# Performance work log

Hardware: AMD Instinct MI355X
Metric: run time of the kernel (lower is better)

The kernel has to match this reference:

```python
import jax, jax.numpy as jnp
import numpy as np

D_MODEL = 1024
N_HEAD = 16
D_K = D_MODEL // N_HEAD
D_FF = 2048
EPS = 1e-6
SCALE = np.sqrt(D_K).astype(np.float32)


def layer_norm(x, alpha, beta):
    # Faithful to source: unbiased std (ddof=1), eps added to std
    mean = jnp.mean(x, axis=-1, keepdims=True)
    std = jnp.std(x, axis=-1, keepdims=True, ddof=1) + EPS
    return alpha * (x - mean) / std + beta


def setup_inputs() -> dict:
    key = jax.random.key(0)
    ks = jax.random.split(key, 12)
    s = 0.02
    return {
        "x": jax.random.normal(ks[0], (4, 1024, D_MODEL), dtype=jnp.float32),
        "Wq": jax.random.normal(ks[1], (D_MODEL, D_MODEL), dtype=jnp.float32) * s,
        "bq": jax.random.normal(ks[2], (D_MODEL,), dtype=jnp.float32) * s,
        "Wo": jax.random.normal(ks[3], (D_MODEL, D_MODEL), dtype=jnp.float32) * s,
        "bo": jax.random.normal(ks[4], (D_MODEL,), dtype=jnp.float32) * s,
        "W1": jax.random.normal(ks[5], (D_MODEL, D_FF), dtype=jnp.float32) * s,
        "b1": jax.random.normal(ks[6], (D_FF,), dtype=jnp.float32) * s,
        "W2": jax.random.normal(ks[7], (D_FF, D_MODEL), dtype=jnp.float32) * s,
        "b2": jax.random.normal(ks[8], (D_MODEL,), dtype=jnp.float32) * s,
        "alpha": jnp.ones((D_MODEL,), dtype=jnp.float32),
        "beta": jnp.ones((D_MODEL,), dtype=jnp.float32),
    }


def reference(x, Wq, bq, Wo, bo, W1, b1, W2, b2, alpha, beta):
    b, s, d = x.shape
    # Source bug kept: q, k, v all use q_linear
    def proj(t):
        return (t @ Wq + bq).reshape(b, s, N_HEAD, D_K).transpose(0, 2, 1, 3)
    q = proj(x)  # [b,h,s,dk]
    k = proj(x)
    v = proj(x)
    scores = jnp.einsum('bhqd,bhkd->bhqk', q, k) / SCALE
    scores = jax.nn.softmax(scores, axis=-1)
    z = jnp.einsum('bhqk,bhkd->bhqd', scores, v)
    concat = z.transpose(0, 2, 1, 3).reshape(b, s, d)
    attn_out = concat @ Wo + bo
    x = layer_norm(x + attn_out, alpha, beta)
    ff = jax.nn.relu(x @ W1 + b1) @ W2 + b2
    x = layer_norm(x + ff, alpha, beta)  # source reuses norm_1
    return x
```

## Files before the change

kernel.cpp:

```cpp
#include <hip/hip_runtime.h>
#include <hip/hip_bf16.h>
#include <stdint.h>

#define TOK   4096
#define DMODEL 1024
#define DFF    2048
#define NHEAD  16
#define DK     64

typedef unsigned short u16;
typedef __attribute__((ext_vector_type(8))) short short8;
typedef __attribute__((ext_vector_type(4))) float f32x4;

typedef __attribute__((address_space(1))) void gvoid;
typedef __attribute__((address_space(3))) void lvoid;

#define QSCALE   0.35355339f
#define QUNSCALE 2.82842712f

__device__ __forceinline__ u16 f2b(float f) {
    uint32_t x = __builtin_bit_cast(uint32_t, f);
    x += 0x7FFFu + ((x >> 16) & 1u);
    return (u16)(x >> 16);
}
__device__ __forceinline__ float b2f(u16 u) {
    uint32_t x = ((uint32_t)u) << 16;
    return __builtin_bit_cast(float, x);
}

__device__ __forceinline__ void gload16(const void* g, void* l) {
    __builtin_amdgcn_global_load_lds((gvoid*)g, (lvoid*)l, 16, 0, 0);
}

__global__ __launch_bounds__(256) void cvt_bf16_k(
    const float* __restrict__ in, u16* __restrict__ out, int n4)
{
    int i = blockIdx.x * 256 + threadIdx.x;
    if (i >= n4) return;
    float4 v = ((const float4*)in)[i];
    ushort4 o;
    o.x = f2b(v.x); o.y = f2b(v.y); o.z = f2b(v.z); o.w = f2b(v.w);
    ((ushort4*)out)[i] = o;
}

__global__ __launch_bounds__(256) void cvt_tr_k(
    const float* __restrict__ W, u16* __restrict__ Wt, int K, int N)
{
    __shared__ u16 T[64][68];
    const int tx = threadIdx.x & 15, ty = threadIdx.x >> 4;
    const int n0 = blockIdx.x * 64, k0 = blockIdx.y * 64;
#pragma unroll
    for (int i = 0; i < 4; i++) {
        int k = ty + i * 16;
        float4 v = *(const float4*)&W[(size_t)(k0 + k) * N + n0 + tx * 4];
        T[tx * 4 + 0][k] = f2b(v.x);
        T[tx * 4 + 1][k] = f2b(v.y);
        T[tx * 4 + 2][k] = f2b(v.z);
        T[tx * 4 + 3][k] = f2b(v.w);
    }
    __syncthreads();
#pragma unroll
    for (int i = 0; i < 4; i++) {
        int n = ty + i * 16;
        ushort4 o;
        o.x = T[n][tx * 4 + 0]; o.y = T[n][tx * 4 + 1];
        o.z = T[n][tx * 4 + 2]; o.w = T[n][tx * 4 + 3];
        *(ushort4*)&Wt[(size_t)(n0 + n) * K + k0 + tx * 4] = o;
    }
}

template<bool RELU, bool OUTBF16, bool QOUT>
__global__ __launch_bounds__(256) void gemm_mfma(
    const u16* __restrict__ A, const u16* __restrict__ Bt,
    const float* __restrict__ bias, void* __restrict__ Cv,
    u16* __restrict__ CT, float oscale,
    int M, int N, int K)
{
    __shared__ __align__(16) u16 As[2 * 128 * 64];
    __shared__ __align__(16) u16 Bs[2 * 128 * 64];

    const int tid  = threadIdx.x;
    const int lane = tid & 63;
    const int wid  = tid >> 6;
    const int wm = wid >> 1, wn = wid & 1;
    const int frow = lane & 15, fk = lane >> 4;

    const int gx = N >> 7;
    const int L = blockIdx.x;
    const int xcd = L & 7, within = L >> 3;
    const int yy = xcd * 4 + within / gx;
    const int xx = within % gx;

    const int row0 = yy * 128;
    const int col0 = xx * 128;

    const u16* gA[4]; u16* lA[4];
    const u16* gB[4]; u16* lB[4];
#pragma unroll
    for (int inst = 0; inst < 4; inst++) {
        int s = inst * 256 + tid;
        int r = s >> 3;
        int kc = ((s & 7) ^ (r & 7)) * 8;
        gA[inst] = A  + (size_t)(row0 + r) * K + kc;
        gB[inst] = Bt + (size_t)(col0 + r) * K + kc;
        lA[inst] = As + inst * 2048 + wid * 512;
        lB[inst] = Bs + inst * 2048 + wid * 512;
    }

    int aoff[4][2], boff[4][2];
#pragma unroll
    for (int m = 0; m < 4; m++) {
        int r = wm * 64 + m * 16 + frow;
#pragma unroll
        for (int kk = 0; kk < 2; kk++)
            aoff[m][kk] = r * 64 + (((kk << 2) + fk) ^ (r & 7)) * 8;
    }
#pragma unroll
    for (int n = 0; n < 4; n++) {
        int r = wn * 64 + n * 16 + frow;
#pragma unroll
        for (int kk = 0; kk < 2; kk++)
            boff[n][kk] = r * 64 + (((kk << 2) + fk) ^ (r & 7)) * 8;
    }

    f32x4 acc[4][4] = {};
    const int nT = K >> 6;

#pragma unroll
    for (int inst = 0; inst < 4; inst++) {
        gload16(gA[inst], lA[inst]);
        gload16(gB[inst], lB[inst]);
    }
    __syncthreads();

    for (int t = 0; t < nT; t++) {
        const int cur = t & 1;
        if (t + 1 < nT) {
            const int k0 = (t + 1) << 6;
            const int bo = (cur ^ 1) * 8192;
#pragma unroll
            for (int inst = 0; inst < 4; inst++) {
                gload16(gA[inst] + k0, lA[inst] + bo);
                gload16(gB[inst] + k0, lB[inst] + bo);
            }
        }

        const u16* Ab = As + cur * 8192;
        const u16* Bb = Bs + cur * 8192;
        short8 a[4][2], b[4][2];
#pragma unroll
        for (int m = 0; m < 4; m++)
#pragma unroll
            for (int kk = 0; kk < 2; kk++)
                a[m][kk] = *(const short8*)(Ab + aoff[m][kk]);
#pragma unroll
        for (int n = 0; n < 4; n++)
#pragma unroll
            for (int kk = 0; kk < 2; kk++)
                b[n][kk] = *(const short8*)(Bb + boff[n][kk]);

#pragma unroll
        for (int m = 0; m < 4; m++)
#pragma unroll
            for (int n = 0; n < 4; n++)
#pragma unroll
                for (int kk = 0; kk < 2; kk++)
                    acc[m][n] = __builtin_amdgcn_mfma_f32_16x16x32_bf16(
                        a[m][kk], b[n][kk], acc[m][n], 0, 0, 0);

        __syncthreads();
    }

#pragma unroll
    for (int n = 0; n < 4; n++) {
        const int gcol = col0 + wn * 64 + n * 16 + frow;
        const float bv = bias[gcol];
#pragma unroll
        for (int m = 0; m < 4; m++) {
            const int grow0 = row0 + wm * 64 + m * 16 + fk * 4;
            float v[4];
#pragma unroll
            for (int i = 0; i < 4; i++) {
                v[i] = (acc[m][n][i] + bv) * oscale;
                if (RELU) v[i] = fmaxf(v[i], 0.0f);
                if (OUTBF16)
                    ((u16*)Cv)[(size_t)(grow0 + i) * N + gcol] = f2b(v[i]);
                else
                    ((float*)Cv)[(size_t)(grow0 + i) * N + gcol] = v[i];
            }
            if (QOUT) {
                const int hh = gcol >> 6, d = gcol & 63;
                const int bb = grow0 >> 10, sl = grow0 & 1023;
                ushort4 o;
                o.x = f2b(v[0]); o.y = f2b(v[1]); o.z = f2b(v[2]); o.w = f2b(v[3]);
                *(ushort4*)&CT[(((size_t)(bb * 16 + hh) * 64 + d) << 10) + sl] = o;
            }
        }
    }
}

__global__ __launch_bounds__(256, 2) void attn_mfma(
    const u16* __restrict__ qb, const u16* __restrict__ qT,
    u16* __restrict__ zb)
{
    __shared__ __align__(16) u16 Ks[2][64 * 64];
    __shared__ __align__(16) u16 Kt[2][64 * 64];
    __shared__ __align__(16) u16 Ps[128 * 64];

    const int tid  = threadIdx.x;
    const int lane = tid & 63;
    const int w    = tid >> 6;
    const int frow = lane & 15, fk = lane >> 4;

    const int h  = blockIdx.x;
    const int qt = blockIdx.y;
    const int b  = blockIdx.z;
    const int q0 = qt * 128;

    const u16* qhead = qb + ((size_t)b * 1024) * 1024 + h * 64;
    const u16* thead = qT + ((size_t)(b * 16 + h) * 64) * 1024;

#pragma unroll
    for (int inst = 0; inst < 2; inst++) {
        int s = inst * 256 + tid, r = s >> 3, kc = ((s & 7) ^ (r & 7)) * 8;
        gload16(qhead + (size_t)r * 1024 + kc, Ks[0] + inst * 2048 + w * 512);
        gload16(thead + (size_t)r * 1024 + kc, Kt[0] + inst * 2048 + w * 512);
    }

    short8 qf[2][2];
#pragma unroll
    for (int m = 0; m < 2; m++) {
        int r = q0 + w * 32 + m * 16 + frow;
#pragma unroll
        for (int kk = 0; kk < 2; kk++)
            qf[m][kk] = *(const short8*)(qhead + (size_t)r * 1024 + kk * 32 + fk * 8);
    }

    float lp[2] = {};
    f32x4 o[2][4] = {};

    __syncthreads();

    for (int t = 0; t < 16; t++) {
        const int cur = t & 1;
        if (t < 15) {
            const int kv = (t + 1) * 64;
#pragma unroll
            for (int inst = 0; inst < 2; inst++) {
                int s = inst * 256 + tid, r = s >> 3, kc = ((s & 7) ^ (r & 7)) * 8;
                gload16(qhead + (size_t)(kv + r) * 1024 + kc,
                        Ks[cur ^ 1] + inst * 2048 + w * 512);
                gload16(thead + (size_t)r * 1024 + kv + kc,
                        Kt[cur ^ 1] + inst * 2048 + w * 512);
            }
        }

        short8 kf[4][2];
#pragma unroll
        for (int n = 0; n < 4; n++) {
            int r = n * 16 + frow;
#pragma unroll
            for (int kk = 0; kk < 2; kk++)
                kf[n][kk] = *(const short8*)(Ks[cur] + r * 64 +
                                             (((kk << 2) + fk) ^ (r & 7)) * 8);
        }
        f32x4 st[4][2] = {};
#pragma unroll
        for (int nk = 0; nk < 4; nk++)
#pragma unroll
            for (int mq = 0; mq < 2; mq++)
#pragma unroll
                for (int kk = 0; kk < 2; kk++)
                    st[nk][mq] = __builtin_amdgcn_mfma_f32_16x16x32_bf16(
                        kf[nk][kk], qf[mq][kk], st[nk][mq], 0, 0, 0);

#pragma unroll
        for (int mq = 0; mq < 2; mq++) {
            const int r = w * 32 + mq * 16 + frow;
            const int rb = r * 64, sw = (r & 7) << 3;
#pragma unroll
            for (int nk = 0; nk < 4; nk++) {
                ushort4 pb;
                float p0 = __expf(st[nk][mq][0]);
                float p1 = __expf(st[nk][mq][1]);
                float p2 = __expf(st[nk][mq][2]);
                float p3 = __expf(st[nk][mq][3]);
                lp[mq] += (p0 + p1) + (p2 + p3);
                pb.x = f2b(p0); pb.y = f2b(p1); pb.z = f2b(p2); pb.w = f2b(p3);
                *(ushort4*)&Ps[rb + ((nk * 16 + fk * 4) ^ sw)] = pb;
            }
        }

        short8 pa[2][2], vf[4][2];
#pragma unroll
        for (int m = 0; m < 2; m++) {
            int r = w * 32 + m * 16 + frow;
#pragma unroll
            for (int kk = 0; kk < 2; kk++)
                pa[m][kk] = *(const short8*)(Ps + r * 64 +
                                             (((kk << 2) + fk) ^ (r & 7)) * 8);
        }
#pragma unroll
        for (int n = 0; n < 4; n++) {
            int r = n * 16 + frow;
#pragma unroll
            for (int kk = 0; kk < 2; kk++)
                vf[n][kk] = *(const short8*)(Kt[cur] + r * 64 +
                                             (((kk << 2) + fk) ^ (r & 7)) * 8);
        }
#pragma unroll
        for (int m = 0; m < 2; m++)
#pragma unroll
            for (int n = 0; n < 4; n++)
#pragma unroll
                for (int kk = 0; kk < 2; kk++)
                    o[m][n] = __builtin_amdgcn_mfma_f32_16x16x32_bf16(
                        pa[m][kk], vf[n][kk], o[m][n], 0, 0, 0);

        __syncthreads();
    }

#pragma unroll
    for (int mq = 0; mq < 2; mq++) {
        lp[mq] += __shfl_xor(lp[mq], 16);
        lp[mq] += __shfl_xor(lp[mq], 32);
    }
#pragma unroll
    for (int m = 0; m < 2; m++)
#pragma unroll
        for (int i = 0; i < 4; i++) {
            const float lfull = __shfl(lp[m], fk * 4 + i);
            const float rl = QUNSCALE / lfull;
            const size_t gr = (size_t)(b * 1024 + q0 + w * 32 + m * 16 + fk * 4 + i);
#pragma unroll
            for (int n = 0; n < 4; n++)
                zb[gr * 1024 + h * 64 + n * 16 + frow] = f2b(o[m][n][i] * rl);
        }
}

__device__ __forceinline__ float ldval(const float* p) { return *p; }
__device__ __forceinline__ float ldval(const u16* p)   { return b2f(*p); }
__device__ __forceinline__ void  stval(float* p, float v) { *p = v; }
__device__ __forceinline__ void  stval(u16* p, float v)   { *p = f2b(v); }

template<typename TA, typename TB, typename TO>
__global__ __launch_bounds__(256) void add_ln(
    const TA* __restrict__ a, const TB* __restrict__ b,
    const float* __restrict__ alpha, const float* __restrict__ beta,
    TO* __restrict__ out)
{
    const int row = blockIdx.x;
    const TA* ar = a + (size_t)row * DMODEL;
    const TB* br = b + (size_t)row * DMODEL;

    float v[4];
    float sum = 0.0f, sq = 0.0f;
#pragma unroll
    for (int i = 0; i < 4; i++) {
        int c = threadIdx.x + i * 256;
        v[i] = ldval(ar + c) + ldval(br + c);
        sum += v[i];
        sq  += v[i] * v[i];
    }
#pragma unroll
    for (int off = 32; off > 0; off >>= 1) {
        sum += __shfl_xor(sum, off);
        sq  += __shfl_xor(sq, off);
    }
    __shared__ float s1[4], s2[4];
    const int wid = threadIdx.x >> 6, lane = threadIdx.x & 63;
    if (lane == 0) { s1[wid] = sum; s2[wid] = sq; }
    __syncthreads();
    sum = s1[0] + s1[1] + s1[2] + s1[3];
    sq  = s2[0] + s2[1] + s2[2] + s2[3];

    const float mean = sum * (1.0f / 1024.0f);
    float var = (sq - 1024.0f * mean * mean) * (1.0f / 1023.0f);
    var = fmaxf(var, 0.0f);
    const float rdenom = 1.0f / (sqrtf(var) + 1e-6f);

#pragma unroll
    for (int i = 0; i < 4; i++) {
        int c = threadIdx.x + i * 256;
        stval(out + (size_t)row * DMODEL + c,
              alpha[c] * (v[i] - mean) * rdenom + beta[c]);
    }
}

extern "C" void kernel_launch(void* const* d_in, const int* in_sizes, int n_in,
                              void* d_out, int out_size, void* d_ws, size_t ws_size,
                              hipStream_t stream) {
    const float* x     = (const float*)d_in[0];
    const float* Wq    = (const float*)d_in[1];
    const float* bq    = (const float*)d_in[2];
    const float* Wo    = (const float*)d_in[3];
    const float* bo    = (const float*)d_in[4];
    const float* W1    = (const float*)d_in[5];
    const float* b1    = (const float*)d_in[6];
    const float* W2    = (const float*)d_in[7];
    const float* b2    = (const float*)d_in[8];
    const float* alpha = (const float*)d_in[9];
    const float* beta  = (const float*)d_in[10];

    char* base = (char*)d_ws;
    u16* Wqt = (u16*)base;
    u16* Wot = (u16*)(base + (2u  << 20));
    u16* W1t = (u16*)(base + (4u  << 20));
    u16* W2t = (u16*)(base + (8u  << 20));
    u16* zb  = (u16*)(base + (12u << 20));
    u16* x1b = zb;
    u16* qb  = (u16*)(base + (20u << 20));
    u16* qT  = (u16*)(base + (28u << 20));
    u16* xb  = (u16*)(base + (36u << 20));
    float* g  = (float*)(base + (36u << 20));
    u16*  hb  = (u16*)g;
    float* g2 = (float*)(base + (20u << 20));

    dim3 blk(256);

    cvt_tr_k<<<dim3(16, 16), blk, 0, stream>>>(Wq, Wqt, 1024, 1024);
    cvt_tr_k<<<dim3(16, 16), blk, 0, stream>>>(Wo, Wot, 1024, 1024);
    cvt_tr_k<<<dim3(32, 16), blk, 0, stream>>>(W1, W1t, 1024, 2048);
    cvt_tr_k<<<dim3(16, 32), blk, 0, stream>>>(W2, W2t, 2048, 1024);
    cvt_bf16_k<<<dim3(TOK * DMODEL / 4 / 256), blk, 0, stream>>>(x, xb, TOK * DMODEL / 4);

    gemm_mfma<false, true, true><<<dim3(8 * 32), blk, 0, stream>>>(
        xb, Wqt, bq, qb, qT, QSCALE, TOK, 1024, 1024);
    attn_mfma<<<dim3(16, 8, 4), blk, 0, stream>>>(qb, qT, zb);
    gemm_mfma<false, false, false><<<dim3(8 * 32), blk, 0, stream>>>(
        zb, Wot, bo, g, nullptr, 1.0f, TOK, 1024, 1024);
    add_ln<float, float, u16><<<dim3(TOK), blk, 0, stream>>>(x, g, alpha, beta, x1b);
    gemm_mfma<true, true, false><<<dim3(16 * 32), blk, 0, stream>>>(
        x1b, W1t, b1, hb, nullptr, 1.0f, TOK, 2048, 1024);
    gemm_mfma<false, false, false><<<dim3(8 * 32), blk, 0, stream>>>(
        hb, W2t, b2, g2, nullptr, 1.0f, TOK, 1024, 2048);
    add_ln<u16, float, float><<<dim3(TOK), blk, 0, stream>>>(
        x1b, g2, alpha, beta, (float*)d_out);
}
```

Baseline: 170.4 us.

## Merge prep kernels, use 128x64 GEMM tiles, bf16 GEMM outputs, vectorize LayerNorm

```diff
diff --git a/kernel.cpp b/kernel.cpp
--- a/kernel.cpp
+++ b/kernel.cpp
@@ -27,28 +27,20 @@
     uint32_t x = ((uint32_t)u) << 16;
     return __builtin_bit_cast(float, x);
 }
+__device__ __forceinline__ uint32_t f2b2(float lo, float hi) {
+    return (uint32_t)f2b(lo) | ((uint32_t)f2b(hi) << 16);
+}
 
 __device__ __forceinline__ void gload16(const void* g, void* l) {
     __builtin_amdgcn_global_load_lds((gvoid*)g, (lvoid*)l, 16, 0, 0);
 }
 
-__global__ __launch_bounds__(256) void cvt_bf16_k(
-    const float* __restrict__ in, u16* __restrict__ out, int n4)
+__device__ __forceinline__ void cvt_tr_dev(
+    const float* __restrict__ W, u16* __restrict__ Wt, int K, int N,
+    int bx, int by, int tid, u16 T[64][68])
 {
-    int i = blockIdx.x * 256 + threadIdx.x;
-    if (i >= n4) return;
-    float4 v = ((const float4*)in)[i];
-    ushort4 o;
-    o.x = f2b(v.x); o.y = f2b(v.y); o.z = f2b(v.z); o.w = f2b(v.w);
-    ((ushort4*)out)[i] = o;
-}
-
-__global__ __launch_bounds__(256) void cvt_tr_k(
-    const float* __restrict__ W, u16* __restrict__ Wt, int K, int N)
-{
-    __shared__ u16 T[64][68];
-    const int tx = threadIdx.x & 15, ty = threadIdx.x >> 4;
-    const int n0 = blockIdx.x * 64, k0 = blockIdx.y * 64;
+    const int tx = tid & 15, ty = tid >> 4;
+    const int n0 = bx * 64, k0 = by * 64;
 #pragma unroll
     for (int i = 0; i < 4; i++) {
         int k = ty + i * 16;
@@ -69,15 +61,48 @@
     }
 }
 
-template<bool RELU, bool OUTBF16, bool QOUT>
+__global__ __launch_bounds__(256) void prep_all(
+    const float* __restrict__ Wq, const float* __restrict__ Wo,
+    const float* __restrict__ W1, const float* __restrict__ W2,
+    u16* __restrict__ Wqt, u16* __restrict__ Wot,
+    u16* __restrict__ W1t, u16* __restrict__ W2t,
+    const float* __restrict__ x, u16* __restrict__ xb)
+{
+    __shared__ u16 T[64][68];
+    const int id = blockIdx.x, tid = threadIdx.x;
+    if (id < 256) {
+        cvt_tr_dev(Wq, Wqt, 1024, 1024, id & 15, id >> 4, tid, T);
+    } else if (id < 512) {
+        int t = id - 256;
+        cvt_tr_dev(Wo, Wot, 1024, 1024, t & 15, t >> 4, tid, T);
+    } else if (id < 1024) {
+        int t = id - 512;
+        cvt_tr_dev(W1, W1t, 1024, 2048, t & 31, t >> 5, tid, T);
+    } else if (id < 1536) {
+        int t = id - 1024;
+        cvt_tr_dev(W2, W2t, 2048, 1024, t & 15, t >> 4, tid, T);
+    } else {
+        size_t base = (size_t)(id - 1536) * 1024 + tid;
+#pragma unroll
+        for (int j = 0; j < 4; j++) {
+            float4 v = ((const float4*)x)[base + j * 256];
+            ((uint2*)xb)[base + j * 256] =
+                make_uint2(f2b2(v.x, v.y), f2b2(v.z, v.w));
+        }
+    }
+}
+
+template<int BN, bool RELU, bool OUTBF16, bool QOUT>
 __global__ __launch_bounds__(256) void gemm_mfma(
     const u16* __restrict__ A, const u16* __restrict__ Bt,
     const float* __restrict__ bias, void* __restrict__ Cv,
     u16* __restrict__ CT, float oscale,
     int M, int N, int K)
 {
+    constexpr int NF = BN / 32;
+    constexpr int BSTR = BN * 64;
     __shared__ __align__(16) u16 As[2 * 128 * 64];
-    __shared__ __align__(16) u16 Bs[2 * 128 * 64];
+    __shared__ __align__(16) u16 Bs[2 * BSTR];
 
     const int tid  = threadIdx.x;
     const int lane = tid & 63;
@@ -85,29 +110,35 @@
     const int wm = wid >> 1, wn = wid & 1;
     const int frow = lane & 15, fk = lane >> 4;
 
-    const int gx = N >> 7;
+    const int gx = N / BN;
     const int L = blockIdx.x;
     const int xcd = L & 7, within = L >> 3;
     const int yy = xcd * 4 + within / gx;
     const int xx = within % gx;
 
     const int row0 = yy * 128;
-    const int col0 = xx * 128;
+    const int col0 = xx * BN;
 
     const u16* gA[4]; u16* lA[4];
-    const u16* gB[4]; u16* lB[4];
+    const u16* gB[NF]; u16* lB[NF];
 #pragma unroll
     for (int inst = 0; inst < 4; inst++) {
         int s = inst * 256 + tid;
         int r = s >> 3;
         int kc = ((s & 7) ^ (r & 7)) * 8;
-        gA[inst] = A  + (size_t)(row0 + r) * K + kc;
+        gA[inst] = A + (size_t)(row0 + r) * K + kc;
+        lA[inst] = As + inst * 2048 + wid * 512;
+    }
+#pragma unroll
+    for (int inst = 0; inst < NF; inst++) {
+        int s = inst * 256 + tid;
+        int r = s >> 3;
+        int kc = ((s & 7) ^ (r & 7)) * 8;
         gB[inst] = Bt + (size_t)(col0 + r) * K + kc;
-        lA[inst] = As + inst * 2048 + wid * 512;
         lB[inst] = Bs + inst * 2048 + wid * 512;
     }
 
-    int aoff[4][2], boff[4][2];
+    int aoff[4][2], boff[NF][2];
 #pragma unroll
     for (int m = 0; m < 4; m++) {
         int r = wm * 64 + m * 16 + frow;
@@ -116,45 +147,44 @@
             aoff[m][kk] = r * 64 + (((kk << 2) + fk) ^ (r & 7)) * 8;
     }
 #pragma unroll
-    for (int n = 0; n < 4; n++) {
-        int r = wn * 64 + n * 16 + frow;
+    for (int n = 0; n < NF; n++) {
+        int r = wn * (BN / 2) + n * 16 + frow;
 #pragma unroll
         for (int kk = 0; kk < 2; kk++)
             boff[n][kk] = r * 64 + (((kk << 2) + fk) ^ (r & 7)) * 8;
     }
 
-    f32x4 acc[4][4] = {};
+    f32x4 acc[4][NF] = {};
     const int nT = K >> 6;
 
 #pragma unroll
-    for (int inst = 0; inst < 4; inst++) {
-        gload16(gA[inst], lA[inst]);
-        gload16(gB[inst], lB[inst]);
-    }
+    for (int inst = 0; inst < 4; inst++) gload16(gA[inst], lA[inst]);
+#pragma unroll
+    for (int inst = 0; inst < NF; inst++) gload16(gB[inst], lB[inst]);
     __syncthreads();
 
     for (int t = 0; t < nT; t++) {
         const int cur = t & 1;
         if (t + 1 < nT) {
             const int k0 = (t + 1) << 6;
-            const int bo = (cur ^ 1) * 8192;
-#pragma unroll
-            for (int inst = 0; inst < 4; inst++) {
-                gload16(gA[inst] + k0, lA[inst] + bo);
-                gload16(gB[inst] + k0, lB[inst] + bo);
-            }
+#pragma unroll
+            for (int inst = 0; inst < 4; inst++)
+                gload16(gA[inst] + k0, lA[inst] + (cur ^ 1) * 8192);
+#pragma unroll
+            for (int inst = 0; inst < NF; inst++)
+                gload16(gB[inst] + k0, lB[inst] + (cur ^ 1) * BSTR);
         }
 
         const u16* Ab = As + cur * 8192;
-        const u16* Bb = Bs + cur * 8192;
-        short8 a[4][2], b[4][2];
+        const u16* Bb = Bs + cur * BSTR;
+        short8 a[4][2], b[NF][2];
 #pragma unroll
         for (int m = 0; m < 4; m++)
 #pragma unroll
             for (int kk = 0; kk < 2; kk++)
                 a[m][kk] = *(const short8*)(Ab + aoff[m][kk]);
 #pragma unroll
-        for (int n = 0; n < 4; n++)
+        for (int n = 0; n < NF; n++)
 #pragma unroll
             for (int kk = 0; kk < 2; kk++)
                 b[n][kk] = *(const short8*)(Bb + boff[n][kk]);
@@ -162,7 +192,7 @@
 #pragma unroll
         for (int m = 0; m < 4; m++)
 #pragma unroll
-            for (int n = 0; n < 4; n++)
+            for (int n = 0; n < NF; n++)
 #pragma unroll
                 for (int kk = 0; kk < 2; kk++)
                     acc[m][n] = __builtin_amdgcn_mfma_f32_16x16x32_bf16(
@@ -172,8 +202,8 @@
     }
 
 #pragma unroll
-    for (int n = 0; n < 4; n++) {
-        const int gcol = col0 + wn * 64 + n * 16 + frow;
+    for (int n = 0; n < NF; n++) {
+        const int gcol = col0 + wn * (BN / 2) + n * 16 + frow;
         const float bv = bias[gcol];
 #pragma unroll
         for (int m = 0; m < 4; m++) {
@@ -191,9 +221,8 @@
             if (QOUT) {
                 const int hh = gcol >> 6, d = gcol & 63;
                 const int bb = grow0 >> 10, sl = grow0 & 1023;
-                ushort4 o;
-                o.x = f2b(v[0]); o.y = f2b(v[1]); o.z = f2b(v[2]); o.w = f2b(v[3]);
-                *(ushort4*)&CT[(((size_t)(bb * 16 + hh) * 64 + d) << 10) + sl] = o;
+                *(uint2*)&CT[(((size_t)(bb * 16 + hh) * 64 + d) << 10) + sl] =
+                    make_uint2(f2b2(v[0], v[1]), f2b2(v[2], v[3]));
             }
         }
     }
@@ -280,14 +309,13 @@
             const int rb = r * 64, sw = (r & 7) << 3;
 #pragma unroll
             for (int nk = 0; nk < 4; nk++) {
-                ushort4 pb;
                 float p0 = __expf(st[nk][mq][0]);
                 float p1 = __expf(st[nk][mq][1]);
                 float p2 = __expf(st[nk][mq][2]);
                 float p3 = __expf(st[nk][mq][3]);
                 lp[mq] += (p0 + p1) + (p2 + p3);
-                pb.x = f2b(p0); pb.y = f2b(p1); pb.z = f2b(p2); pb.w = f2b(p3);
-                *(ushort4*)&Ps[rb + ((nk * 16 + fk * 4) ^ sw)] = pb;
+                *(uint2*)&Ps[rb + ((nk * 16 + fk * 4) ^ sw)] =
+                    make_uint2(f2b2(p0, p1), f2b2(p2, p3));
             }
         }
 
@@ -338,10 +366,15 @@
         }
 }
 
-__device__ __forceinline__ float ldval(const float* p) { return *p; }
-__device__ __forceinline__ float ldval(const u16* p)   { return b2f(*p); }
-__device__ __forceinline__ void  stval(float* p, float v) { *p = v; }
-__device__ __forceinline__ void  stval(u16* p, float v)   { *p = f2b(v); }
+__device__ __forceinline__ float4 ld4(const float* p) { return *(const float4*)p; }
+__device__ __forceinline__ float4 ld4(const u16* p) {
+    ushort4 u = *(const ushort4*)p;
+    return make_float4(b2f(u.x), b2f(u.y), b2f(u.z), b2f(u.w));
+}
+__device__ __forceinline__ void st4(float* p, float4 v) { *(float4*)p = v; }
+__device__ __forceinline__ void st4(u16* p, float4 v) {
+    *(uint2*)p = make_uint2(f2b2(v.x, v.y), f2b2(v.z, v.w));
+}
 
 template<typename TA, typename TB, typename TO>
 __global__ __launch_bounds__(256) void add_ln(
@@ -350,18 +383,14 @@
     TO* __restrict__ out)
 {
     const int row = blockIdx.x;
-    const TA* ar = a + (size_t)row * DMODEL;
-    const TB* br = b + (size_t)row * DMODEL;
-
-    float v[4];
-    float sum = 0.0f, sq = 0.0f;
-#pragma unroll
-    for (int i = 0; i < 4; i++) {
-        int c = threadIdx.x + i * 256;
-        v[i] = ldval(ar + c) + ldval(br + c);
-        sum += v[i];
-        sq  += v[i] * v[i];
-    }
+    const int c = threadIdx.x * 4;
+    float4 va = ld4(a + (size_t)row * DMODEL + c);
+    float4 vb = ld4(b + (size_t)row * DMODEL + c);
+    float v0 = va.x + vb.x, v1 = va.y + vb.y;
+    float v2 = va.z + vb.z, v3 = va.w + vb.w;
+
+    float sum = (v0 + v1) + (v2 + v3);
+    float sq  = (v0 * v0 + v1 * v1) + (v2 * v2 + v3 * v3);
 #pragma unroll
     for (int off = 32; off > 0; off >>= 1) {
         sum += __shfl_xor(sum, off);
@@ -371,20 +400,22 @@
     const int wid = threadIdx.x >> 6, lane = threadIdx.x & 63;
     if (lane == 0) { s1[wid] = sum; s2[wid] = sq; }
     __syncthreads();
-    sum = s1[0] + s1[1] + s1[2] + s1[3];
-    sq  = s2[0] + s2[1] + s2[2] + s2[3];
+    sum = (s1[0] + s1[1]) + (s1[2] + s1[3]);
+    sq  = (s2[0] + s2[1]) + (s2[2] + s2[3]);
 
     const float mean = sum * (1.0f / 1024.0f);
     float var = (sq - 1024.0f * mean * mean) * (1.0f / 1023.0f);
     var = fmaxf(var, 0.0f);
     const float rdenom = 1.0f / (sqrtf(var) + 1e-6f);
 
-#pragma unroll
-    for (int i = 0; i < 4; i++) {
-        int c = threadIdx.x + i * 256;
-        stval(out + (size_t)row * DMODEL + c,
-              alpha[c] * (v[i] - mean) * rdenom + beta[c]);
-    }
+    float4 al = *(const float4*)(alpha + c);
+    float4 be = *(const float4*)(beta + c);
+    float4 r;
+    r.x = al.x * (v0 - mean) * rdenom + be.x;
+    r.y = al.y * (v1 - mean) * rdenom + be.y;
+    r.z = al.z * (v2 - mean) * rdenom + be.z;
+    r.w = al.w * (v3 - mean) * rdenom + be.w;
+    st4(out + (size_t)row * DMODEL + c, r);
 }
 
 extern "C" void kernel_launch(void* const* d_in, const int* in_sizes, int n_in,
@@ -410,30 +441,27 @@
     u16* zb  = (u16*)(base + (12u << 20));
     u16* x1b = zb;
     u16* qb  = (u16*)(base + (20u << 20));
+    u16* g2  = qb;
     u16* qT  = (u16*)(base + (28u << 20));
     u16* xb  = (u16*)(base + (36u << 20));
-    float* g  = (float*)(base + (36u << 20));
-    u16*  hb  = (u16*)g;
-    float* g2 = (float*)(base + (20u << 20));
+    u16* g   = xb;
+    u16* hb  = (u16*)(base + (36u << 20));
 
     dim3 blk(256);
 
-    cvt_tr_k<<<dim3(16, 16), blk, 0, stream>>>(Wq, Wqt, 1024, 1024);
-    cvt_tr_k<<<dim3(16, 16), blk, 0, stream>>>(Wo, Wot, 1024, 1024);
-    cvt_tr_k<<<dim3(32, 16), blk, 0, stream>>>(W1, W1t, 1024, 2048);
-    cvt_tr_k<<<dim3(16, 32), blk, 0, stream>>>(W2, W2t, 2048, 1024);
-    cvt_bf16_k<<<dim3(TOK * DMODEL / 4 / 256), blk, 0, stream>>>(x, xb, TOK * DMODEL / 4);
-
-    gemm_mfma<false, true, true><<<dim3(8 * 32), blk, 0, stream>>>(
+    prep_all<<<dim3(2560), blk, 0, stream>>>(
+        Wq, Wo, W1, W2, Wqt, Wot, W1t, W2t, x, xb);
+
+    gemm_mfma<64, false, true, true><<<dim3(512), blk, 0, stream>>>(
         xb, Wqt, bq, qb, qT, QSCALE, TOK, 1024, 1024);
     attn_mfma<<<dim3(16, 8, 4), blk, 0, stream>>>(qb, qT, zb);
-    gemm_mfma<false, false, false><<<dim3(8 * 32), blk, 0, stream>>>(
+    gemm_mfma<64, false, true, false><<<dim3(512), blk, 0, stream>>>(
         zb, Wot, bo, g, nullptr, 1.0f, TOK, 1024, 1024);
-    add_ln<float, float, u16><<<dim3(TOK), blk, 0, stream>>>(x, g, alpha, beta, x1b);
-    gemm_mfma<true, true, false><<<dim3(16 * 32), blk, 0, stream>>>(
+    add_ln<float, u16, u16><<<dim3(TOK), blk, 0, stream>>>(x, g, alpha, beta, x1b);
+    gemm_mfma<128, true, true, false><<<dim3(512), blk, 0, stream>>>(
         x1b, W1t, b1, hb, nullptr, 1.0f, TOK, 2048, 1024);
-    gemm_mfma<false, false, false><<<dim3(8 * 32), blk, 0, stream>>>(
+    gemm_mfma<64, false, true, false><<<dim3(512), blk, 0, stream>>>(
         hb, W2t, b2, g2, nullptr, 1.0f, TOK, 1024, 2048);
-    add_ln<u16, float, float><<<dim3(TOK), blk, 0, stream>>>(
+    add_ln<u16, u16, float><<<dim3(TOK), blk, 0, stream>>>(
         x1b, g2, alpha, beta, (float*)d_out);
 }
```

After: 146.4 us. 1.16x faster.
